# Kernel optimization log

Hardware: AMD Instinct MI355X
Metric: run time of the kernel (lower is better)

## Reference

```python
import jax, jax.numpy as jnp
import numpy as np

B1, B2, R, L, D, H = 48, 48, 36, 30, 1024, 4
EPS = 1e-8


def _l2norm(x):
    return x / (jnp.sqrt(jnp.sum(x * x, axis=-1, keepdims=True)) + EPS)


def _summary_attn(x, w1, b1, w2, b2):
    # x: (B1,B2,N,D). MLP scores -> softmax over N -> weighted mean over H heads.
    h = jax.nn.relu(jnp.einsum('abnd,ed->abne', x, w1) + b1)
    s = jnp.einsum('abne,he->abnh', h, w2) + b2          # (B1,B2,N,H)
    p = jax.nn.softmax(jnp.swapaxes(s, -1, -2), axis=-1)  # (B1,B2,H,N)
    w = jnp.einsum('abhn,abnd->abhd', p, x)               # (B1,B2,H,D)
    return w.mean(axis=-2)                                # (B1,B2,D)


def setup_inputs() -> dict:
    key = jax.random.key(0)
    ks = jax.random.split(key, 12)
    r = np.sqrt(6.0) / np.sqrt(D + D)  # xavier uniform as in init_weights
    return {
        'v1': jax.random.normal(ks[0], (B1, R, D), dtype=jnp.float32),
        'v2': jax.random.normal(ks[1], (B2, L, D), dtype=jnp.float32),
        'w_img': jax.random.uniform(ks[2], (D, D), jnp.float32, -r, r),
        'w_txt': jax.random.uniform(ks[3], (D, D), jnp.float32, -r, r),
        'w1a': jax.random.normal(ks[4], (D, D), jnp.float32) * 0.02,
        'b1a': jnp.zeros((D,), jnp.float32),
        'w2a': jax.random.normal(ks[5], (H, D), jnp.float32) * 0.02,
        'b2a': jnp.zeros((H,), jnp.float32),
        'w1b': jax.random.normal(ks[6], (D, D), jnp.float32) * 0.02,
        'b1b': jnp.zeros((D,), jnp.float32),
        'w2b': jax.random.normal(ks[7], (H, D), jnp.float32) * 0.02,
        'b2b': jnp.zeros((H,), jnp.float32),
    }


def reference(v1, v2, w_img, w_txt, w1a, b1a, w2a, b2a, w1b, b1b, w2b, b2b):
    d = v1.shape[-1]
    inv_sqrt_d = np.float32(1.0 / np.sqrt(d))
    k1 = jnp.einsum('ard,ed->are', v1, w_img)  # (B1,R,D)
    k2 = jnp.einsum('bld,ed->ble', v2, w_txt)  # (B2,L,D)

    # qkv_attention(k2, k1, v1): queries=words, keys/values=regions
    s1 = jnp.einsum('bld,ard->ablr', k2, k1) * inv_sqrt_d   # (B1,B2,L,R)
    p1 = jax.nn.softmax(s1, axis=-1)
    fused_v2 = jnp.einsum('ablr,ard->abld', p1, v1)         # weighted_v1 -> fused_v2

    # qkv_attention(k1, k2, v2): queries=regions, keys/values=words
    s2 = jnp.einsum('ard,bld->abrl', k1, k2) * inv_sqrt_d   # (B1,B2,R,L)
    p2 = jax.nn.softmax(s2, axis=-1)
    fused_v1 = jnp.einsum('abrl,bld->abrd', p2, v2)         # weighted_v2 -> fused_v1

    co_v1 = _l2norm(_summary_attn(fused_v1, w1a, b1a, w2a, b2a))
    co_v2 = _l2norm(_summary_attn(fused_v2, w1b, b1b, w2b, b2b))
    return jnp.sum(co_v1 * co_v2, axis=-1)  # (B1,B2) score matrix
```

## Files before the change

kernel.cpp:

```cpp
#include <hip/hip_runtime.h>

#define D 1024
#define NB1 48
#define NB2 48
#define RR 36
#define LL 30
#define NH 4

typedef short bf16x8 __attribute__((ext_vector_type(8)));
typedef float f32x4 __attribute__((ext_vector_type(4)));
typedef float f32x2 __attribute__((ext_vector_type(2)));
typedef unsigned short u16x8 __attribute__((ext_vector_type(8)));

#define MFMA16(a, b, c) __builtin_amdgcn_mfma_f32_16x16x32_bf16(a, b, c, 0, 0, 0)

__device__ __forceinline__ unsigned short f2bf(float x) {
  unsigned u = __float_as_uint(x);
  u += 0x7FFF + ((u >> 16) & 1);
  return (unsigned short)(u >> 16);
}
__device__ __forceinline__ float bf2f(unsigned short h) {
  return __uint_as_float(((unsigned)h) << 16);
}
__device__ __forceinline__ void split8(const float* v, bf16x8& h8, bf16x8& l8) {
  u16x8 hi, lo;
#pragma unroll
  for (int i = 0; i < 8; ++i) {
    unsigned short h = f2bf(v[i]);
    hi[i] = h;
    lo[i] = f2bf(v[i] - bf2f(h));
  }
  h8 = __builtin_bit_cast(bf16x8, hi);
  l8 = __builtin_bit_cast(bf16x8, lo);
}
__device__ __forceinline__ f32x2 shflx2(f32x2 v, int m) {
  double d = __builtin_bit_cast(double, v);
  d = __shfl_xor(d, m);
  return __builtin_bit_cast(f32x2, d);
}

__device__ __forceinline__ void conv_body(const float* __restrict__ X,
                                          unsigned short* __restrict__ out,
                                          int rows, int g) {
  const int lane = threadIdx.x & 63;
  const int tile = g >> 5, kc = g & 31;
  const int row = tile * 16 + (lane & 15);
  const int k = kc * 32 + (lane >> 4) * 8;
  float v[8];
  if (row < rows) {
    const float4* s = (const float4*)(X + (size_t)row * 1024 + k);
    float4 x0 = s[0], x1 = s[1];
    v[0] = x0.x; v[1] = x0.y; v[2] = x0.z; v[3] = x0.w;
    v[4] = x1.x; v[5] = x1.y; v[6] = x1.z; v[7] = x1.w;
  } else {
#pragma unroll
    for (int i = 0; i < 8; ++i) v[i] = 0.f;
  }
  bf16x8 hi, lo;
  split8(v, hi, lo);
  bf16x8* o = (bf16x8*)(out + (size_t)g * 1024 + lane * 8);
  o[0] = hi;
  o[64] = lo;
}

__global__ __launch_bounds__(256) void conv6(
    const float* __restrict__ v1, const float* __restrict__ v2,
    const float* __restrict__ wimg, const float* __restrict__ wtxt,
    const float* __restrict__ w1a, const float* __restrict__ w1b,
    unsigned short* v1f, unsigned short* v2f, unsigned short* wimgf,
    unsigned short* wtxtf, unsigned short* w1af, unsigned short* w1bf) {
  const float* X; unsigned short* O; int rows;
  switch (blockIdx.y) {
    case 0: X = v1; O = v1f; rows = 1728; break;
    case 1: X = v2; O = v2f; rows = 1440; break;
    case 2: X = wimg; O = wimgf; rows = 1024; break;
    case 3: X = wtxt; O = wtxtf; rows = 1024; break;
    case 4: X = w1a; O = w1af; rows = 1024; break;
    default: X = w1b; O = w1bf; rows = 1024; break;
  }
  const int tiles = (rows + 15) >> 4;
  const int g = blockIdx.x * 4 + (threadIdx.x >> 6);
  if (g >= tiles * 32) return;
  conv_body(X, O, rows, g);
}

__global__ __launch_bounds__(256) void conv_k(const float* __restrict__ k1,
                                              const float* __restrict__ k2,
                                              unsigned short* k1f, unsigned short* k2f) {
  const float* X = blockIdx.y ? k2 : k1;
  unsigned short* O = blockIdx.y ? k2f : k1f;
  const int rows = blockIdx.y ? 1440 : 1728;
  const int tiles = (rows + 15) >> 4;
  const int g = blockIdx.x * 4 + (threadIdx.x >> 6);
  if (g >= tiles * 32) return;
  conv_body(X, O, rows, g);
}

__global__ __launch_bounds__(256) void convG(const float* __restrict__ G2a,
                                             const float* __restrict__ G1b,
                                             const float* __restrict__ w2a,
                                             const float* __restrict__ w2b,
                                             unsigned short* G2aF, unsigned short* G1bF,
                                             float4* __restrict__ w2at,
                                             float4* __restrict__ w2bt) {
  const int t = threadIdx.x, lane = t & 63;
  if (blockIdx.y == 0 && blockIdx.x < 4) {
    int col = blockIdx.x * 256 + t;
    w2at[col] = make_float4(w2a[col], w2a[1024 + col], w2a[2048 + col], w2a[3072 + col]);
    w2bt[col] = make_float4(w2b[col], w2b[1024 + col], w2b[2048 + col], w2b[3072 + col]);
  }
  const int bb = blockIdx.x >> 4;
  const int nt = ((blockIdx.x & 15) << 2) + (t >> 6);
  const int c = lane & 15, q = lane >> 4;
  if (blockIdx.y == 0) {
    float v[8];
#pragma unroll
    for (int j = 0; j < 8; ++j) {
      int l = q * 8 + j;
      v[j] = (l < LL) ? G2a[(size_t)(bb * LL + l) * D + nt * 16 + c] : 0.f;
    }
    bf16x8 hi, lo;
    split8(v, hi, lo);
    bf16x8* o = (bf16x8*)(G2aF + ((size_t)(bb * 64 + nt) * 2) * 512 + lane * 8);
    o[0] = hi;
    o[64] = lo;
  } else {
#pragma unroll
    for (int kc = 0; kc < 2; ++kc) {
      float v[8];
#pragma unroll
      for (int j = 0; j < 8; ++j) {
        int r = kc * 32 + q * 8 + j;
        v[j] = (r < RR) ? G1b[(size_t)(bb * RR + r) * D + nt * 16 + c] : 0.f;
      }
      bf16x8 hi, lo;
      split8(v, hi, lo);
      bf16x8* o = (bf16x8*)(G1bF + (((size_t)(bb * 64 + nt) * 2 + kc) * 2) * 512 + lane * 8);
      o[0] = hi;
      o[64] = lo;
    }
  }
}

__device__ __forceinline__ void gemm4_body(const bf16x8* __restrict__ Af,
                                           const bf16x8* __restrict__ Bf,
                                           float* __restrict__ C,
                                           int M, int N, float scale,
                                           int Mtiles, int Ntiles) {
  const int lane = threadIdx.x & 63;
  const int w = threadIdx.x >> 6;
  const int mb = blockIdx.y * 8 + (w >> 1) * 4;
  const int nb = blockIdx.x * 8 + (w & 1) * 4;
  size_t ab[4], bb[4];
#pragma unroll
  for (int i = 0; i < 4; ++i) {
    int tm = mb + i; if (tm > Mtiles - 1) tm = Mtiles - 1;
    ab[i] = (size_t)tm * 4096 + lane;
    int tn = nb + i; if (tn > Ntiles - 1) tn = Ntiles - 1;
    bb[i] = (size_t)tn * 4096 + lane;
  }
  f32x4 acc[4][4];
#pragma unroll
  for (int i = 0; i < 4; ++i)
#pragma unroll
    for (int j = 0; j < 4; ++j) acc[i][j] = (f32x4){0.f, 0.f, 0.f, 0.f};
#pragma unroll 1
  for (int kc = 0; kc < 32; ++kc) {
    bf16x8 ah[4], al[4], bh[4], bl[4];
#pragma unroll
    for (int i = 0; i < 4; ++i) { ah[i] = Af[ab[i]]; al[i] = Af[ab[i] + 64]; ab[i] += 128; }
#pragma unroll
    for (int j = 0; j < 4; ++j) { bh[j] = Bf[bb[j]]; bl[j] = Bf[bb[j] + 64]; bb[j] += 128; }
#pragma unroll
    for (int i = 0; i < 4; ++i)
#pragma unroll
      for (int j = 0; j < 4; ++j) {
        acc[i][j] = MFMA16(ah[i], bh[j], acc[i][j]);
        acc[i][j] = MFMA16(al[i], bh[j], acc[i][j]);
        acc[i][j] = MFMA16(ah[i], bl[j], acc[i][j]);
      }
  }
  const int c16 = lane & 15, q = lane >> 4;
#pragma unroll
  for (int i = 0; i < 4; ++i) {
#pragma unroll
    for (int reg = 0; reg < 4; ++reg) {
      int r = (mb + i) * 16 + q * 4 + reg;
      if (r < M) {
#pragma unroll
        for (int j = 0; j < 4; ++j) {
          int col = (nb + j) * 16 + c16;
          if (col < N) C[(size_t)r * N + col] = acc[i][j][reg] * scale;
        }
      }
    }
  }
}

__global__ __launch_bounds__(256) void proj_fused(
    const bf16x8* __restrict__ v1f, const bf16x8* __restrict__ v2f,
    const bf16x8* __restrict__ wimgf, const bf16x8* __restrict__ wtxtf,
    const bf16x8* __restrict__ w1af, const bf16x8* __restrict__ w1bf,
    float* k1, float* k2, float* G2a, float* G1b) {
  const int z = blockIdx.z;
  const bf16x8* Af = (z == 0 || z == 3) ? v1f : v2f;
  const bf16x8* Bf = (z == 0) ? wimgf : (z == 1) ? wtxtf : (z == 2) ? w1af : w1bf;
  float* C = (z == 0) ? k1 : (z == 1) ? k2 : (z == 2) ? G2a : G1b;
  const int M = (z == 0 || z == 3) ? 1728 : 1440;
  const int Mt = (z == 0 || z == 3) ? 108 : 92;
  if ((int)blockIdx.y * 8 >= Mt) return;
  gemm4_body(Af, Bf, C, M, 1024, 1.f, Mt, 64);
}

__global__ __launch_bounds__(256) void cross_fused(
    const bf16x8* __restrict__ k2f, const bf16x8* __restrict__ k1f,
    const bf16x8* __restrict__ v2f, const bf16x8* __restrict__ v1f,
    float* Sbuf, float* Cbuf) {
  if (blockIdx.z == 0) gemm4_body(k2f, k1f, Sbuf, 1440, 1728, 0.03125f, 92, 108);
  else                 gemm4_body(v2f, v1f, Cbuf, 1440, 1728, 1.f, 92, 108);
}

__global__ __launch_bounds__(256) void gram_partial(const float* __restrict__ v1,
                                                    const float* __restrict__ v2,
                                                    float* __restrict__ pg) {
  const int y = blockIdx.y, cx = blockIdx.x;
  const int isV1 = y < 48;
  const int batch = isV1 ? y : y - 48;
  const int Nr = isV1 ? RR : LL;
  const float* base = isV1 ? v1 + (size_t)batch * RR * D : v2 + (size_t)batch * LL * D;
  __shared__ __align__(16) float vs[36][132];
  const int t = threadIdx.x;
  for (int idx = t; idx < Nr * 32; idx += 256) {
    int row = idx >> 5, c4 = idx & 31;
    *(float4*)&vs[row][c4 * 4] = *(const float4*)&base[(size_t)row * D + cx * 128 + c4 * 4];
  }
  __syncthreads();
  const int nt3 = Nr / 3;
  float acc[3][3] = {{0.f,0.f,0.f},{0.f,0.f,0.f},{0.f,0.f,0.f}};
  const int i0 = (t / nt3) * 3, j0 = (t - (t / nt3) * nt3) * 3;
  if (t < nt3 * nt3) {
    for (int k4 = 0; k4 < 32; ++k4) {
      float4 a[3], b[3];
#pragma unroll
      for (int ii = 0; ii < 3; ++ii) a[ii] = *(const float4*)&vs[i0 + ii][k4 * 4];
#pragma unroll
      for (int jj = 0; jj < 3; ++jj) b[jj] = *(const float4*)&vs[j0 + jj][k4 * 4];
#pragma unroll
      for (int ii = 0; ii < 3; ++ii)
#pragma unroll
        for (int jj = 0; jj < 3; ++jj) {
          acc[ii][jj] = fmaf(a[ii].x, b[jj].x, acc[ii][jj]);
          acc[ii][jj] = fmaf(a[ii].y, b[jj].y, acc[ii][jj]);
          acc[ii][jj] = fmaf(a[ii].z, b[jj].z, acc[ii][jj]);
          acc[ii][jj] = fmaf(a[ii].w, b[jj].w, acc[ii][jj]);
        }
    }
    float* o = pg + ((size_t)y * 8 + cx) * 1296;
#pragma unroll
    for (int ii = 0; ii < 3; ++ii)
#pragma unroll
      for (int jj = 0; jj < 3; ++jj) o[(i0 + ii) * Nr + (j0 + jj)] = acc[ii][jj];
  }
}

__global__ __launch_bounds__(256) void gram_reduce(const float* __restrict__ pg,
                                                   float* __restrict__ g11,
                                                   float* __restrict__ g22) {
  const int y = blockIdx.x;
  const int isV1 = y < 48;
  const int batch = isV1 ? y : y - 48;
  const int NN = isV1 ? RR * RR : LL * LL;
  const float* p = pg + (size_t)y * 8 * 1296;
  float* o = isV1 ? g11 + (size_t)batch * RR * RR : g22 + (size_t)batch * LL * LL;
  for (int i = threadIdx.x; i < NN; i += 256) {
    float s = 0.f;
#pragma unroll
    for (int c = 0; c < 8; ++c) s += p[c * 1296 + i];
    o[i] = s;
  }
}

__global__ __launch_bounds__(128) void pair_dir(
    const float* __restrict__ Sb,
    const bf16x8* __restrict__ G2aF, const bf16x8* __restrict__ G1bF,
    const float* __restrict__ g22, const float* __restrict__ g11,
    const float* __restrict__ b1a, const float4* __restrict__ w2at, const float* __restrict__ b2a,
    const float* __restrict__ b1b, const float4* __restrict__ w2bt, const float* __restrict__ b2b,
    float* __restrict__ U1buf, float* __restrict__ U2buf,
    float* __restrict__ N1buf, float* __restrict__ N2buf) {
  const int pair = blockIdx.x;
  const int a = pair / NB2;
  const int b = pair - a * NB2;
  const int t = threadIdx.x, lane = t & 63, w = t >> 6;
  const int c16 = lane & 15, q = lane >> 4;

  union SM {
    struct {
      float p2s[48][36];
      float red[2][48][4];
      float sa[RR][NH];
      float qa[RR];
      float u2[LL];
      float rb[2];
    } A;
    struct {
      float p1s[32][68];
      float red[2][48][4];
      float sbm[LL][NH];
      float qb[LL];
      float u1[RR];
      float rb[2];
    } B;
  };
  __shared__ __align__(16) SM sm;

  const float* Sab = Sb + (size_t)b * LL * 1728 + (size_t)a * RR;

  if (blockIdx.y == 0) {
    for (int i = t; i < 48 * 36; i += 128) {
      int r = i / 36, c = i - r * 36;
      if (r >= RR || c >= LL) ((float*)sm.A.p2s)[i] = 0.f;
    }
    for (int i = t; i < LL * RR; i += 128) {
      int l = i / RR, r = i - l * RR;
      sm.A.p2s[r][l] = Sab[(size_t)l * 1728 + r];
    }
    __syncthreads();
    if (t < RR * 2) {
      int r = t >> 1, half = t & 1;
      float m = -1e30f;
      for (int l = half; l < LL; l += 2) m = fmaxf(m, sm.A.p2s[r][l]);
      m = fmaxf(m, __shfl_xor(m, 1));
      float s = 0.f;
      for (int l = half; l < LL; l += 2) {
        float e = __expf(sm.A.p2s[r][l] - m);
        sm.A.p2s[r][l] = e;
        s += e;
      }
      s += __shfl_xor(s, 1);
      float inv = 1.f / s;
      for (int l = half; l < LL; l += 2) sm.A.p2s[r][l] *= inv;
    }
    __syncthreads();

    bf16x8 pAh[3], pAl[3];
#pragma unroll
    for (int mt = 0; mt < 3; ++mt) {
      float v[8];
      const float* rp = &sm.A.p2s[mt * 16 + c16][q * 8];
      float4 x0 = *(const float4*)rp;
      float4 x1 = *(const float4*)(rp + 4);
      v[0] = x0.x; v[1] = x0.y; v[2] = x0.z; v[3] = x0.w;
      v[4] = x1.x; v[5] = x1.y; v[6] = x1.z; v[7] = x1.w;
      split8(v, pAh[mt], pAl[mt]);
    }

    f32x2 sc01[3][4], sc23[3][4];
#pragma unroll
    for (int mt = 0; mt < 3; ++mt)
#pragma unroll
      for (int reg = 0; reg < 4; ++reg) {
        sc01[mt][reg] = (f32x2){0.f, 0.f};
        sc23[mt][reg] = (f32x2){0.f, 0.f};
      }

    const bf16x8* gA = G2aF + ((size_t)(b * 64 + w) * 2) * 64 + lane;
#pragma unroll 2
    for (int it = 0; it < 32; ++it) {
      const bf16x8* gp = gA + (size_t)it * 256;
      bf16x8 Bh = gp[0], Bl = gp[64];
      const int col = (w + it * 2) * 16 + c16;
      float4 wv = w2at[col];
      float bias = b1a[col];
      f32x2 w01 = {wv.x, wv.y}, w23 = {wv.z, wv.w};
#pragma unroll
      for (int mt = 0; mt < 3; ++mt) {
        f32x4 acc = {bias, bias, bias, bias};
        acc = MFMA16(pAh[mt], Bh, acc);
        acc = MFMA16(pAl[mt], Bh, acc);
        acc = MFMA16(pAh[mt], Bl, acc);
#pragma unroll
        for (int reg = 0; reg < 4; ++reg) {
          float hv = fmaxf(acc[reg], 0.f);
          f32x2 hv2 = {hv, hv};
          sc01[mt][reg] += hv2 * w01;
          sc23[mt][reg] += hv2 * w23;
        }
      }
    }
#pragma unroll
    for (int mt = 0; mt < 3; ++mt)
#pragma unroll
      for (int reg = 0; reg < 4; ++reg) {
        f32x2 v01 = sc01[mt][reg], v23 = sc23[mt][reg];
#pragma unroll
        for (int m = 1; m <= 8; m <<= 1) {
          v01 += shflx2(v01, m);
          v23 += shflx2(v23, m);
        }
        if (c16 == 0) {
          f32x2* rp = (f32x2*)&sm.A.red[w][mt * 16 + q * 4 + reg][0];
          rp[0] = v01;
          rp[1] = v23;
        }
      }
    __syncthreads();
    for (int i = t; i < RR * NH; i += 128) {
      int r = i >> 2, h = i & 3;
      sm.A.sa[r][h] = sm.A.red[0][r][h] + sm.A.red[1][r][h] + b2a[h];
    }
    __syncthreads();
    if (t < 64) {
      const int h = t >> 4, i = t & 15;
      float x0 = sm.A.sa[i][h];
      float x1 = sm.A.sa[i + 16][h];
      float x2 = (i < 4) ? sm.A.sa[i + 32][h] : -1e30f;
      float m = fmaxf(fmaxf(x0, x1), x2);
      m = fmaxf(m, __shfl_xor(m, 1));
      m = fmaxf(m, __shfl_xor(m, 2));
      m = fmaxf(m, __shfl_xor(m, 4));
      m = fmaxf(m, __shfl_xor(m, 8));
      float e0 = __expf(x0 - m), e1 = __expf(x1 - m);
      float e2 = (i < 4) ? __expf(x2 - m) : 0.f;
      float s = e0 + e1 + e2;
      s += __shfl_xor(s, 1);
      s += __shfl_xor(s, 2);
      s += __shfl_xor(s, 4);
      s += __shfl_xor(s, 8);
      float inv = 1.f / s;
      sm.A.sa[i][h] = e0 * inv;
      sm.A.sa[i + 16][h] = e1 * inv;
      if (i < 4) sm.A.sa[i + 32][h] = e2 * inv;
    }
    __syncthreads();
    if (t < RR)
      sm.A.qa[t] = 0.25f * (sm.A.sa[t][0] + sm.A.sa[t][1] + sm.A.sa[t][2] + sm.A.sa[t][3]);
    __syncthreads();
    if (t < LL * 2) {
      int l = t >> 1, half = t & 1;
      float x = 0.f;
      for (int r = half; r < RR; r += 2) x = fmaf(sm.A.qa[r], sm.A.p2s[r][l], x);
      x += __shfl_xor(x, 1);
      if (half == 0) {
        sm.A.u2[l] = x;
        U2buf[pair * 32 + l] = x;
      }
    }
    __syncthreads();
    float pn1 = 0.f;
    const float* G22 = g22 + (size_t)b * LL * LL;
    for (int i = t; i < LL * LL; i += 128) {
      int l = i / LL, l2 = i - l * LL;
      pn1 = fmaf(sm.A.u2[l] * sm.A.u2[l2], G22[i], pn1);
    }
#pragma unroll
    for (int off = 32; off; off >>= 1) pn1 += __shfl_down(pn1, off);
    if (lane == 0) sm.A.rb[w] = pn1;
    __syncthreads();
    if (t == 0) N1buf[pair] = sm.A.rb[0] + sm.A.rb[1];
  } else {
    for (int i = t; i < 32 * 68; i += 128) {
      int l = i / 68, c = i - l * 68;
      if (l >= LL || c >= RR) ((float*)sm.B.p1s)[i] = 0.f;
    }
    for (int i = t; i < LL * RR; i += 128) {
      int l = i / RR, r = i - l * RR;
      sm.B.p1s[l][r] = Sab[(size_t)l * 1728 + r];
    }
    __syncthreads();
    if (t < LL * 2) {
      int l = t >> 1, half = t & 1;
      float m = -1e30f;
      for (int r = half; r < RR; r += 2) m = fmaxf(m, sm.B.p1s[l][r]);
      m = fmaxf(m, __shfl_xor(m, 1));
      float s = 0.f;
      for (int r = half; r < RR; r += 2) {
        float e = __expf(sm.B.p1s[l][r] - m);
        sm.B.p1s[l][r] = e;
        s += e;
      }
      s += __shfl_xor(s, 1);
      float inv = 1.f / s;
      for (int r = half; r < RR; r += 2) sm.B.p1s[l][r] *= inv;
    }
    __syncthreads();

    bf16x8 pBh[2][2], pBl[2][2];
#pragma unroll
    for (int mt = 0; mt < 2; ++mt)
#pragma unroll
      for (int kc = 0; kc < 2; ++kc) {
        float v[8];
        const float* rp = &sm.B.p1s[mt * 16 + c16][kc * 32 + q * 8];
        float4 x0 = *(const float4*)rp;
        float4 x1 = *(const float4*)(rp + 4);
        v[0] = x0.x; v[1] = x0.y; v[2] = x0.z; v[3] = x0.w;
        v[4] = x1.x; v[5] = x1.y; v[6] = x1.z; v[7] = x1.w;
        split8(v, pBh[mt][kc], pBl[mt][kc]);
      }

    f32x2 sc01[2][4], sc23[2][4];
#pragma unroll
    for (int mt = 0; mt < 2; ++mt)
#pragma unroll
      for (int reg = 0; reg < 4; ++reg) {
        sc01[mt][reg] = (f32x2){0.f, 0.f};
        sc23[mt][reg] = (f32x2){0.f, 0.f};
      }

    const bf16x8* gB = G1bF + ((size_t)(a * 64 + w) * 4) * 64 + lane;
#pragma unroll 2
    for (int it = 0; it < 32; ++it) {
      const bf16x8* gp = gB + (size_t)it * 512;
      bf16x8 B0h = gp[0], B0l = gp[64], B1h = gp[128], B1l = gp[192];
      const int col = (w + it * 2) * 16 + c16;
      float4 wv = w2bt[col];
      float bias = b1b[col];
      f32x2 w01 = {wv.x, wv.y}, w23 = {wv.z, wv.w};
#pragma unroll
      for (int mt = 0; mt < 2; ++mt) {
        f32x4 acc = {bias, bias, bias, bias};
        acc = MFMA16(pBh[mt][0], B0h, acc);
        acc = MFMA16(pBl[mt][0], B0h, acc);
        acc = MFMA16(pBh[mt][0], B0l, acc);
        acc = MFMA16(pBh[mt][1], B1h, acc);
        acc = MFMA16(pBl[mt][1], B1h, acc);
        acc = MFMA16(pBh[mt][1], B1l, acc);
#pragma unroll
        for (int reg = 0; reg < 4; ++reg) {
          float hv = fmaxf(acc[reg], 0.f);
          f32x2 hv2 = {hv, hv};
          sc01[mt][reg] += hv2 * w01;
          sc23[mt][reg] += hv2 * w23;
        }
      }
    }
#pragma unroll
    for (int mt = 0; mt < 2; ++mt)
#pragma unroll
      for (int reg = 0; reg < 4; ++reg) {
        f32x2 v01 = sc01[mt][reg], v23 = sc23[mt][reg];
#pragma unroll
        for (int m = 1; m <= 8; m <<= 1) {
          v01 += shflx2(v01, m);
          v23 += shflx2(v23, m);
        }
        if (c16 == 0) {
          f32x2* rp = (f32x2*)&sm.B.red[w][mt * 16 + q * 4 + reg][0];
          rp[0] = v01;
          rp[1] = v23;
        }
      }
    __syncthreads();
    for (int i = t; i < LL * NH; i += 128) {
      int l = i >> 2, h = i & 3;
      sm.B.sbm[l][h] = sm.B.red[0][l][h] + sm.B.red[1][l][h] + b2b[h];
    }
    __syncthreads();
    if (t < 64) {
      const int h = t >> 4, i = t & 15;
      float x0 = sm.B.sbm[i][h];
      float x1 = (i < 14) ? sm.B.sbm[i + 16][h] : -1e30f;
      float m = fmaxf(x0, x1);
      m = fmaxf(m, __shfl_xor(m, 1));
      m = fmaxf(m, __shfl_xor(m, 2));
      m = fmaxf(m, __shfl_xor(m, 4));
      m = fmaxf(m, __shfl_xor(m, 8));
      float e0 = __expf(x0 - m);
      float e1 = (i < 14) ? __expf(x1 - m) : 0.f;
      float s = e0 + e1;
      s += __shfl_xor(s, 1);
      s += __shfl_xor(s, 2);
      s += __shfl_xor(s, 4);
      s += __shfl_xor(s, 8);
      float inv = 1.f / s;
      sm.B.sbm[i][h] = e0 * inv;
      if (i < 14) sm.B.sbm[i + 16][h] = e1 * inv;
    }
    __syncthreads();
    if (t < LL)
      sm.B.qb[t] = 0.25f * (sm.B.sbm[t][0] + sm.B.sbm[t][1] + sm.B.sbm[t][2] + sm.B.sbm[t][3]);
    __syncthreads();
    if (t < RR * 2) {
      int r = t >> 1, half = t & 1;
      float x = 0.f;
      for (int l = half; l < LL; l += 2) x = fmaf(sm.B.qb[l], sm.B.p1s[l][r], x);
      x += __shfl_xor(x, 1);
      if (half == 0) {
        sm.B.u1[r] = x;
        U1buf[pair * 40 + r] = x;
      }
    }
    __syncthreads();
    float pn2 = 0.f;
    const float* G11 = g11 + (size_t)a * RR * RR;
    for (int i = t; i < RR * RR; i += 128) {
      int r = i / RR, r2 = i - r * RR;
      pn2 = fmaf(sm.B.u1[r] * sm.B.u1[r2], G11[i], pn2);
    }
#pragma unroll
    for (int off = 32; off; off >>= 1) pn2 += __shfl_down(pn2, off);
    if (lane == 0) sm.B.rb[w] = pn2;
    __syncthreads();
    if (t == 0) N2buf[pair] = sm.B.rb[0] + sm.B.rb[1];
  }
}

__global__ __launch_bounds__(64) void pair_final(
    const float* __restrict__ Cb, const float* __restrict__ U1buf,
    const float* __restrict__ U2buf, const float* __restrict__ N1buf,
    const float* __restrict__ N2buf, float* __restrict__ out) {
  const int pair = blockIdx.x;
  const int a = pair / NB2;
  const int b = pair - a * NB2;
  const int t = threadIdx.x;
  const float* Cab = Cb + (size_t)b * LL * 1728 + (size_t)a * RR;
  const float* u1 = U1buf + pair * 40;
  const float* u2 = U2buf + pair * 32;
  float pnum = 0.f;
  for (int i = t; i < LL * RR; i += 64) {
    int l = i / RR, r = i - l * RR;
    pnum = fmaf(u2[l] * u1[r], Cab[(size_t)l * 1728 + r], pnum);
  }
#pragma unroll
  for (int off = 32; off; off >>= 1) pnum += __shfl_down(pnum, off);
  if (t == 0) {
    float n1 = sqrtf(fmaxf(N1buf[pair], 0.f));
    float n2 = sqrtf(fmaxf(N2buf[pair], 0.f));
    out[pair] = pnum / ((n1 + 1e-8f) * (n2 + 1e-8f));
  }
}

extern "C" void kernel_launch(void* const* d_in, const int* in_sizes, int n_in,
                              void* d_out, int out_size, void* d_ws, size_t ws_size,
                              hipStream_t stream) {
  const float* v1    = (const float*)d_in[0];
  const float* v2    = (const float*)d_in[1];
  const float* w_img = (const float*)d_in[2];
  const float* w_txt = (const float*)d_in[3];
  const float* w1a   = (const float*)d_in[4];
  const float* b1a   = (const float*)d_in[5];
  const float* w2a   = (const float*)d_in[6];
  const float* b2a   = (const float*)d_in[7];
  const float* w1b   = (const float*)d_in[8];
  const float* b1b   = (const float*)d_in[9];
  const float* w2b   = (const float*)d_in[10];
  const float* b2b   = (const float*)d_in[11];
  float* out = (float*)d_out;

  float* ws   = (float*)d_ws;
  float* k1   = ws;
  float* k2   = k1 + (size_t)1728 * 1024;
  float* G2a  = k2 + (size_t)1440 * 1024;
  float* G1b  = G2a + (size_t)1440 * 1024;
  float* Sbuf = G1b + (size_t)1728 * 1024;
  float* Cbuf = Sbuf + (size_t)1440 * 1728;
  float* g22  = Cbuf + (size_t)1440 * 1728;
  float* g11  = g22 + (size_t)48 * 900;

  unsigned short* fb    = (unsigned short*)(g11 + (size_t)48 * 1296);
  unsigned short* v1f   = fb;
  unsigned short* v2f   = v1f + (size_t)108 * 32768;
  unsigned short* k1f   = v2f + (size_t)92 * 32768;
  unsigned short* k2f   = k1f + (size_t)108 * 32768;
  unsigned short* wimgf = k2f + (size_t)92 * 32768;
  unsigned short* wtxtf = wimgf + (size_t)64 * 32768;
  unsigned short* w1af  = wtxtf + (size_t)64 * 32768;
  unsigned short* w1bf  = w1af + (size_t)64 * 32768;
  unsigned short* G2aF  = w1bf + (size_t)64 * 32768;
  unsigned short* G1bF  = G2aF + (size_t)48 * 65536;

  float* pg = (float*)k1f;

  float4* w2at = (float4*)k1;
  float4* w2bt = w2at + 1024;

  float* U2buf = G2a;
  float* U1buf = U2buf + (size_t)2304 * 32;
  float* N1buf = U1buf + (size_t)2304 * 40;
  float* N2buf = N1buf + 2304;

  conv6<<<dim3(864, 6), 256, 0, stream>>>(v1, v2, w_img, w_txt, w1a, w1b,
                                          v1f, v2f, wimgf, wtxtf, w1af, w1bf);
  gram_partial<<<dim3(8, 96), 256, 0, stream>>>(v1, v2, pg);
  gram_reduce<<<96, 256, 0, stream>>>(pg, g11, g22);

  proj_fused<<<dim3(8, 14, 4), 256, 0, stream>>>(
      (const bf16x8*)v1f, (const bf16x8*)v2f, (const bf16x8*)wimgf,
      (const bf16x8*)wtxtf, (const bf16x8*)w1af, (const bf16x8*)w1bf,
      k1, k2, G2a, G1b);

  conv_k<<<dim3(864, 2), 256, 0, stream>>>(k1, k2, k1f, k2f);
  convG<<<dim3(768, 2), 256, 0, stream>>>(G2a, G1b, w2a, w2b, G2aF, G1bF, w2at, w2bt);

  cross_fused<<<dim3(14, 12, 2), 256, 0, stream>>>(
      (const bf16x8*)k2f, (const bf16x8*)k1f, (const bf16x8*)v2f, (const bf16x8*)v1f,
      Sbuf, Cbuf);

  pair_dir<<<dim3(2304, 2), 128, 0, stream>>>(
      Sbuf, (const bf16x8*)G2aF, (const bf16x8*)G1bF, g22, g11,
      b1a, w2at, b2a, b1b, w2bt, b2b, U1buf, U2buf, N1buf, N2buf);
  pair_final<<<2304, 64, 0, stream>>>(Cbuf, U1buf, U2buf, N1buf, N2buf, out);
}
```

Measured before the change: 310.0 us.

## Replace Gram and cross-value GEMMs with per-pair summary vectors; double-buffer GEMM loads

The Gram-matrix kernels and the v2·v1ᵀ cross GEMM are removed. Each pair now builds its D-dim summary vectors directly as u-weighted sums of the v2 and v1 rows, writes them out, and computes their squared norms. pair_final then takes a 1024-length dot product instead of a weighted sum over the cross matrix. This drops half of cross_fused and two launches, but adds per-pair reads of v1/v2 rows (L2-resident) and 2304×1024×2 float writes. gemm4_body also gains register double-buffering of fragment loads and 32-bit offsets.

```diff
diff --git a/kernel.cpp b/kernel.cpp
--- a/kernel.cpp
+++ b/kernel.cpp
@@ -142,6 +142,24 @@
   }
 }
 
+#define LOAD_FRAGS(AH, AL, BH, BL)                                              \
+  {                                                                             \
+    _Pragma("unroll") for (int i = 0; i < 4; ++i) {                             \
+      AH[i] = Af[ab[i]]; AL[i] = Af[ab[i] + 64]; ab[i] += 128;                  \
+    }                                                                           \
+    _Pragma("unroll") for (int j = 0; j < 4; ++j) {                             \
+      BH[j] = Bf[bb[j]]; BL[j] = Bf[bb[j] + 64]; bb[j] += 128;                  \
+    }                                                                           \
+  }
+
+#define MFMA_SET(AH, AL, BH, BL)                                                \
+  _Pragma("unroll") for (int i = 0; i < 4; ++i)                                 \
+      _Pragma("unroll") for (int j = 0; j < 4; ++j) {                           \
+    acc[i][j] = MFMA16(AH[i], BH[j], acc[i][j]);                                \
+    acc[i][j] = MFMA16(AL[i], BH[j], acc[i][j]);                                \
+    acc[i][j] = MFMA16(AH[i], BL[j], acc[i][j]);                                \
+  }
+
 __device__ __forceinline__ void gemm4_body(const bf16x8* __restrict__ Af,
                                            const bf16x8* __restrict__ Bf,
                                            float* __restrict__ C,
@@ -151,35 +169,34 @@
   const int w = threadIdx.x >> 6;
   const int mb = blockIdx.y * 8 + (w >> 1) * 4;
   const int nb = blockIdx.x * 8 + (w & 1) * 4;
-  size_t ab[4], bb[4];
+  int ab[4], bb[4];
 #pragma unroll
   for (int i = 0; i < 4; ++i) {
     int tm = mb + i; if (tm > Mtiles - 1) tm = Mtiles - 1;
-    ab[i] = (size_t)tm * 4096 + lane;
+    ab[i] = tm * 4096 + lane;
     int tn = nb + i; if (tn > Ntiles - 1) tn = Ntiles - 1;
-    bb[i] = (size_t)tn * 4096 + lane;
+    bb[i] = tn * 4096 + lane;
   }
   f32x4 acc[4][4];
 #pragma unroll
   for (int i = 0; i < 4; ++i)
 #pragma unroll
     for (int j = 0; j < 4; ++j) acc[i][j] = (f32x4){0.f, 0.f, 0.f, 0.f};
+
+  bf16x8 ahA[4], alA[4], bhA[4], blA[4];
+  bf16x8 ahB[4], alB[4], bhB[4], blB[4];
+  LOAD_FRAGS(ahA, alA, bhA, blA);
 #pragma unroll 1
-  for (int kc = 0; kc < 32; ++kc) {
-    bf16x8 ah[4], al[4], bh[4], bl[4];
-#pragma unroll
-    for (int i = 0; i < 4; ++i) { ah[i] = Af[ab[i]]; al[i] = Af[ab[i] + 64]; ab[i] += 128; }
-#pragma unroll
-    for (int j = 0; j < 4; ++j) { bh[j] = Bf[bb[j]]; bl[j] = Bf[bb[j] + 64]; bb[j] += 128; }
-#pragma unroll
-    for (int i = 0; i < 4; ++i)
-#pragma unroll
-      for (int j = 0; j < 4; ++j) {
-        acc[i][j] = MFMA16(ah[i], bh[j], acc[i][j]);
-        acc[i][j] = MFMA16(al[i], bh[j], acc[i][j]);
-        acc[i][j] = MFMA16(ah[i], bl[j], acc[i][j]);
-      }
-  }
+  for (int kc = 0; kc < 30; kc += 2) {
+    LOAD_FRAGS(ahB, alB, bhB, blB);
+    MFMA_SET(ahA, alA, bhA, blA);
+    LOAD_FRAGS(ahA, alA, bhA, blA);
+    MFMA_SET(ahB, alB, bhB, blB);
+  }
+  LOAD_FRAGS(ahB, alB, bhB, blB);
+  MFMA_SET(ahA, alA, bhA, blA);
+  MFMA_SET(ahB, alB, bhB, blB);
+
   const int c16 = lane & 15, q = lane >> 4;
 #pragma unroll
   for (int i = 0; i < 4; ++i) {
@@ -212,81 +229,19 @@
   gemm4_body(Af, Bf, C, M, 1024, 1.f, Mt, 64);
 }
 
-__global__ __launch_bounds__(256) void cross_fused(
+__global__ __launch_bounds__(256) void cross_s(
     const bf16x8* __restrict__ k2f, const bf16x8* __restrict__ k1f,
-    const bf16x8* __restrict__ v2f, const bf16x8* __restrict__ v1f,
-    float* Sbuf, float* Cbuf) {
-  if (blockIdx.z == 0) gemm4_body(k2f, k1f, Sbuf, 1440, 1728, 0.03125f, 92, 108);
-  else                 gemm4_body(v2f, v1f, Cbuf, 1440, 1728, 1.f, 92, 108);
-}
-
-__global__ __launch_bounds__(256) void gram_partial(const float* __restrict__ v1,
-                                                    const float* __restrict__ v2,
-                                                    float* __restrict__ pg) {
-  const int y = blockIdx.y, cx = blockIdx.x;
-  const int isV1 = y < 48;
-  const int batch = isV1 ? y : y - 48;
-  const int Nr = isV1 ? RR : LL;
-  const float* base = isV1 ? v1 + (size_t)batch * RR * D : v2 + (size_t)batch * LL * D;
-  __shared__ __align__(16) float vs[36][132];
-  const int t = threadIdx.x;
-  for (int idx = t; idx < Nr * 32; idx += 256) {
-    int row = idx >> 5, c4 = idx & 31;
-    *(float4*)&vs[row][c4 * 4] = *(const float4*)&base[(size_t)row * D + cx * 128 + c4 * 4];
-  }
-  __syncthreads();
-  const int nt3 = Nr / 3;
-  float acc[3][3] = {{0.f,0.f,0.f},{0.f,0.f,0.f},{0.f,0.f,0.f}};
-  const int i0 = (t / nt3) * 3, j0 = (t - (t / nt3) * nt3) * 3;
-  if (t < nt3 * nt3) {
-    for (int k4 = 0; k4 < 32; ++k4) {
-      float4 a[3], b[3];
-#pragma unroll
-      for (int ii = 0; ii < 3; ++ii) a[ii] = *(const float4*)&vs[i0 + ii][k4 * 4];
-#pragma unroll
-      for (int jj = 0; jj < 3; ++jj) b[jj] = *(const float4*)&vs[j0 + jj][k4 * 4];
-#pragma unroll
-      for (int ii = 0; ii < 3; ++ii)
-#pragma unroll
-        for (int jj = 0; jj < 3; ++jj) {
-          acc[ii][jj] = fmaf(a[ii].x, b[jj].x, acc[ii][jj]);
-          acc[ii][jj] = fmaf(a[ii].y, b[jj].y, acc[ii][jj]);
-          acc[ii][jj] = fmaf(a[ii].z, b[jj].z, acc[ii][jj]);
-          acc[ii][jj] = fmaf(a[ii].w, b[jj].w, acc[ii][jj]);
-        }
-    }
-    float* o = pg + ((size_t)y * 8 + cx) * 1296;
-#pragma unroll
-    for (int ii = 0; ii < 3; ++ii)
-#pragma unroll
-      for (int jj = 0; jj < 3; ++jj) o[(i0 + ii) * Nr + (j0 + jj)] = acc[ii][jj];
-  }
-}
-
-__global__ __launch_bounds__(256) void gram_reduce(const float* __restrict__ pg,
-                                                   float* __restrict__ g11,
-                                                   float* __restrict__ g22) {
-  const int y = blockIdx.x;
-  const int isV1 = y < 48;
-  const int batch = isV1 ? y : y - 48;
-  const int NN = isV1 ? RR * RR : LL * LL;
-  const float* p = pg + (size_t)y * 8 * 1296;
-  float* o = isV1 ? g11 + (size_t)batch * RR * RR : g22 + (size_t)batch * LL * LL;
-  for (int i = threadIdx.x; i < NN; i += 256) {
-    float s = 0.f;
-#pragma unroll
-    for (int c = 0; c < 8; ++c) s += p[c * 1296 + i];
-    o[i] = s;
-  }
+    float* Sbuf) {
+  gemm4_body(k2f, k1f, Sbuf, 1440, 1728, 0.03125f, 92, 108);
 }
 
 __global__ __launch_bounds__(128) void pair_dir(
     const float* __restrict__ Sb,
+    const float* __restrict__ v1, const float* __restrict__ v2,
     const bf16x8* __restrict__ G2aF, const bf16x8* __restrict__ G1bF,
-    const float* __restrict__ g22, const float* __restrict__ g11,
     const float* __restrict__ b1a, const float4* __restrict__ w2at, const float* __restrict__ b2a,
     const float* __restrict__ b1b, const float4* __restrict__ w2bt, const float* __restrict__ b2b,
-    float* __restrict__ U1buf, float* __restrict__ U2buf,
+    float* __restrict__ YA, float* __restrict__ YB,
     float* __restrict__ N1buf, float* __restrict__ N2buf) {
   const int pair = blockIdx.x;
   const int a = pair / NB2;
@@ -441,23 +396,32 @@
       float x = 0.f;
       for (int r = half; r < RR; r += 2) x = fmaf(sm.A.qa[r], sm.A.p2s[r][l], x);
       x += __shfl_xor(x, 1);
-      if (half == 0) {
-        sm.A.u2[l] = x;
-        U2buf[pair * 32 + l] = x;
-      }
-    }
-    __syncthreads();
-    float pn1 = 0.f;
-    const float* G22 = g22 + (size_t)b * LL * LL;
-    for (int i = t; i < LL * LL; i += 128) {
-      int l = i / LL, l2 = i - l * LL;
-      pn1 = fmaf(sm.A.u2[l] * sm.A.u2[l2], G22[i], pn1);
-    }
-#pragma unroll
-    for (int off = 32; off; off >>= 1) pn1 += __shfl_down(pn1, off);
-    if (lane == 0) sm.A.rb[w] = pn1;
-    __syncthreads();
-    if (t == 0) N1buf[pair] = sm.A.rb[0] + sm.A.rb[1];
+      if (half == 0) sm.A.u2[l] = x;
+    }
+    __syncthreads();
+    {
+      const float* V2b = v2 + ((size_t)b * LL) * D + t * 8;
+      float4 y0 = {0.f, 0.f, 0.f, 0.f}, y1 = {0.f, 0.f, 0.f, 0.f};
+      for (int l = 0; l < LL; ++l) {
+        float ul = sm.A.u2[l];
+        float4 aa = *(const float4*)(V2b + (size_t)l * D);
+        float4 cc = *(const float4*)(V2b + (size_t)l * D + 4);
+        y0.x = fmaf(ul, aa.x, y0.x); y0.y = fmaf(ul, aa.y, y0.y);
+        y0.z = fmaf(ul, aa.z, y0.z); y0.w = fmaf(ul, aa.w, y0.w);
+        y1.x = fmaf(ul, cc.x, y1.x); y1.y = fmaf(ul, cc.y, y1.y);
+        y1.z = fmaf(ul, cc.z, y1.z); y1.w = fmaf(ul, cc.w, y1.w);
+      }
+      float4* Yo = (float4*)(YA + (size_t)pair * 1024 + t * 8);
+      Yo[0] = y0;
+      Yo[1] = y1;
+      float pn1 = y0.x * y0.x + y0.y * y0.y + y0.z * y0.z + y0.w * y0.w +
+                  y1.x * y1.x + y1.y * y1.y + y1.z * y1.z + y1.w * y1.w;
+#pragma unroll
+      for (int off = 32; off; off >>= 1) pn1 += __shfl_down(pn1, off);
+      if (lane == 0) sm.A.rb[w] = pn1;
+      __syncthreads();
+      if (t == 0) N1buf[pair] = sm.A.rb[0] + sm.A.rb[1];
+    }
   } else {
     for (int i = t; i < 32 * 68; i += 128) {
       int l = i / 68, c = i - l * 68;
@@ -586,48 +550,59 @@
       float x = 0.f;
       for (int l = half; l < LL; l += 2) x = fmaf(sm.B.qb[l], sm.B.p1s[l][r], x);
       x += __shfl_xor(x, 1);
-      if (half == 0) {
-        sm.B.u1[r] = x;
-        U1buf[pair * 40 + r] = x;
-      }
-    }
-    __syncthreads();
-    float pn2 = 0.f;
-    const float* G11 = g11 + (size_t)a * RR * RR;
-    for (int i = t; i < RR * RR; i += 128) {
-      int r = i / RR, r2 = i - r * RR;
-      pn2 = fmaf(sm.B.u1[r] * sm.B.u1[r2], G11[i], pn2);
-    }
-#pragma unroll
-    for (int off = 32; off; off >>= 1) pn2 += __shfl_down(pn2, off);
-    if (lane == 0) sm.B.rb[w] = pn2;
-    __syncthreads();
-    if (t == 0) N2buf[pair] = sm.B.rb[0] + sm.B.rb[1];
-  }
-}
-
-__global__ __launch_bounds__(64) void pair_final(
-    const float* __restrict__ Cb, const float* __restrict__ U1buf,
-    const float* __restrict__ U2buf, const float* __restrict__ N1buf,
-    const float* __restrict__ N2buf, float* __restrict__ out) {
+      if (half == 0) sm.B.u1[r] = x;
+    }
+    __syncthreads();
+    {
+      const float* V1a = v1 + ((size_t)a * RR) * D + t * 8;
+      float4 y0 = {0.f, 0.f, 0.f, 0.f}, y1 = {0.f, 0.f, 0.f, 0.f};
+      for (int r = 0; r < RR; ++r) {
+        float ur = sm.B.u1[r];
+        float4 aa = *(const float4*)(V1a + (size_t)r * D);
+        float4 cc = *(const float4*)(V1a + (size_t)r * D + 4);
+        y0.x = fmaf(ur, aa.x, y0.x); y0.y = fmaf(ur, aa.y, y0.y);
+        y0.z = fmaf(ur, aa.z, y0.z); y0.w = fmaf(ur, aa.w, y0.w);
+        y1.x = fmaf(ur, cc.x, y1.x); y1.y = fmaf(ur, cc.y, y1.y);
+        y1.z = fmaf(ur, cc.z, y1.z); y1.w = fmaf(ur, cc.w, y1.w);
+      }
+      float4* Yo = (float4*)(YB + (size_t)pair * 1024 + t * 8);
+      Yo[0] = y0;
+      Yo[1] = y1;
+      float pn2 = y0.x * y0.x + y0.y * y0.y + y0.z * y0.z + y0.w * y0.w +
+                  y1.x * y1.x + y1.y * y1.y + y1.z * y1.z + y1.w * y1.w;
+#pragma unroll
+      for (int off = 32; off; off >>= 1) pn2 += __shfl_down(pn2, off);
+      if (lane == 0) sm.B.rb[w] = pn2;
+      __syncthreads();
+      if (t == 0) N2buf[pair] = sm.B.rb[0] + sm.B.rb[1];
+    }
+  }
+}
+
+__global__ __launch_bounds__(128) void pair_final(
+    const float* __restrict__ YA, const float* __restrict__ YB,
+    const float* __restrict__ N1buf, const float* __restrict__ N2buf,
+    float* __restrict__ out) {
   const int pair = blockIdx.x;
-  const int a = pair / NB2;
-  const int b = pair - a * NB2;
   const int t = threadIdx.x;
-  const float* Cab = Cb + (size_t)b * LL * 1728 + (size_t)a * RR;
-  const float* u1 = U1buf + pair * 40;
-  const float* u2 = U2buf + pair * 32;
-  float pnum = 0.f;
-  for (int i = t; i < LL * RR; i += 64) {
-    int l = i / RR, r = i - l * RR;
-    pnum = fmaf(u2[l] * u1[r], Cab[(size_t)l * 1728 + r], pnum);
-  }
-#pragma unroll
-  for (int off = 32; off; off >>= 1) pnum += __shfl_down(pnum, off);
+  const float4* ya = (const float4*)(YA + (size_t)pair * 1024);
+  const float4* yb = (const float4*)(YB + (size_t)pair * 1024);
+  float s = 0.f;
+#pragma unroll
+  for (int i = 0; i < 2; ++i) {
+    float4 a = ya[t + i * 128], b = yb[t + i * 128];
+    s += a.x * b.x + a.y * b.y + a.z * b.z + a.w * b.w;
+  }
+#pragma unroll
+  for (int off = 32; off; off >>= 1) s += __shfl_down(s, off);
+  __shared__ float r2[2];
+  if ((t & 63) == 0) r2[t >> 6] = s;
+  __syncthreads();
   if (t == 0) {
+    float num = r2[0] + r2[1];
     float n1 = sqrtf(fmaxf(N1buf[pair], 0.f));
     float n2 = sqrtf(fmaxf(N2buf[pair], 0.f));
-    out[pair] = pnum / ((n1 + 1e-8f) * (n2 + 1e-8f));
+    out[pair] = num / ((n1 + 1e-8f) * (n2 + 1e-8f));
   }
 }
 
@@ -657,6 +632,7 @@
   float* Cbuf = Sbuf + (size_t)1440 * 1728;
   float* g22  = Cbuf + (size_t)1440 * 1728;
   float* g11  = g22 + (size_t)48 * 900;
+  (void)g22; (void)g11;
 
   unsigned short* fb    = (unsigned short*)(g11 + (size_t)48 * 1296);
   unsigned short* v1f   = fb;
@@ -670,20 +646,16 @@
   unsigned short* G2aF  = w1bf + (size_t)64 * 32768;
   unsigned short* G1bF  = G2aF + (size_t)48 * 65536;
 
-  float* pg = (float*)k1f;
-
   float4* w2at = (float4*)k1;
   float4* w2bt = w2at + 1024;
 
-  float* U2buf = G2a;
-  float* U1buf = U2buf + (size_t)2304 * 32;
-  float* N1buf = U1buf + (size_t)2304 * 40;
+  float* YA = Cbuf;
+  float* YB = (float*)k1f;
+  float* N1buf = G2a;
   float* N2buf = N1buf + 2304;
 
   conv6<<<dim3(864, 6), 256, 0, stream>>>(v1, v2, w_img, w_txt, w1a, w1b,
                                           v1f, v2f, wimgf, wtxtf, w1af, w1bf);
-  gram_partial<<<dim3(8, 96), 256, 0, stream>>>(v1, v2, pg);
-  gram_reduce<<<96, 256, 0, stream>>>(pg, g11, g22);
 
   proj_fused<<<dim3(8, 14, 4), 256, 0, stream>>>(
       (const bf16x8*)v1f, (const bf16x8*)v2f, (const bf16x8*)wimgf,
@@ -693,12 +665,11 @@
   conv_k<<<dim3(864, 2), 256, 0, stream>>>(k1, k2, k1f, k2f);
   convG<<<dim3(768, 2), 256, 0, stream>>>(G2a, G1b, w2a, w2b, G2aF, G1bF, w2at, w2bt);
 
-  cross_fused<<<dim3(14, 12, 2), 256, 0, stream>>>(
-      (const bf16x8*)k2f, (const bf16x8*)k1f, (const bf16x8*)v2f, (const bf16x8*)v1f,
-      Sbuf, Cbuf);
+  cross_s<<<dim3(14, 12), 256, 0, stream>>>(
+      (const bf16x8*)k2f, (const bf16x8*)k1f, Sbuf);
 
   pair_dir<<<dim3(2304, 2), 128, 0, stream>>>(
-      Sbuf, (const bf16x8*)G2aF, (const bf16x8*)G1bF, g22, g11,
-      b1a, w2at, b2a, b1b, w2bt, b2b, U1buf, U2buf, N1buf, N2buf);
-  pair_final<<<2304, 64, 0, stream>>>(Cbuf, U1buf, U2buf, N1buf, N2buf, out);
-}
+      Sbuf, v1, v2, (const bf16x8*)G2aF, (const bf16x8*)G1bF,
+      b1a, w2at, b2a, b1b, w2bt, b2b, YA, YB, N1buf, N2buf);
+  pair_final<<<2304, 128, 0, stream>>>(YA, YB, N1buf, N2buf, out);
+}
```

Result: no change. 313.2 us (+1.0%).
